# Kernel tuning notes

Hardware: AMD Instinct MI355X
Metric: run time of the kernel (lower is better)

## Reference

```python
import jax, jax.numpy as jnp
import numpy as np

B, S, D, H = 4, 4096, 1024, 16
DH = D // H


def setup_inputs() -> dict:
    key = jax.random.key(0)
    ks = jax.random.split(key, 8)
    scale = 1.0 / np.sqrt(D)
    return {
        "q": jax.random.normal(ks[0], (B, S, D), jnp.float32),
        "k": jax.random.normal(ks[1], (B, S, D), jnp.float32),
        "v": jax.random.normal(ks[2], (B, S, D), jnp.float32),
        "mask": jax.random.uniform(ks[3], (H, H), jnp.float32),
        # torch nn.Linear weights, layout [out, in]; applied as x @ W.T
        "Wq": jax.random.normal(ks[4], (D, D), jnp.float32) * scale,
        "Wk": jax.random.normal(ks[5], (D, D), jnp.float32) * scale,
        "Wv": jax.random.normal(ks[6], (D, D), jnp.float32) * scale,
        "Wo": jax.random.normal(ks[7], (D, D), jnp.float32) * scale,
    }


def reference(q, k, v, mask, Wq, Wk, Wv, Wo):
    # projections (bias-free Linear): x @ W.T, then split to [B,S,H,DH]
    qh = (q @ Wq.T).reshape(B, S, H, DH)
    kh = (k @ Wk.T).reshape(B, S, H, DH)
    vh = (v @ Wv.T).reshape(B, S, H, DH)
    # Faithful to source: NO head/seq transpose, so attention is over the
    # head axis per token: score [B,S,H,H]
    score = jnp.einsum('bshd,bsgd->bshg', qh, kh) / np.sqrt(DH)
    score = score * mask  # multiplicative mask, broadcast [H,H]
    p = jax.nn.softmax(score, axis=-1)
    attn = jnp.einsum('bshg,bsgd->bshd', p, vh)  # [B,S,H,DH]
    out = attn.reshape(B, S, D) @ Wo.T
    return out
```

## Files before the change

### kernel.cpp

```cpp
#include <hip/hip_runtime.h>
#include <hip/hip_bf16.h>
#include <stdint.h>


namespace {
constexpr int kD  = 1024;
constexpr int kH  = 16;
constexpr int kDH = 64;
constexpr int kM  = 4 * 4096;
constexpr size_t PER = (size_t)kM * kD;
constexpr size_t WSZ = (size_t)kD * kD;

typedef __attribute__((ext_vector_type(4))) float f32x4;
typedef __attribute__((ext_vector_type(8))) short s16x8;

__device__ __forceinline__ unsigned short f2b(float f) {
  uint32_t x = __builtin_bit_cast(uint32_t, f);
  x += 0x7fffu + ((x >> 16) & 1u);
  return (unsigned short)(x >> 16);
}
__device__ __forceinline__ float b2f(unsigned short u) {
  return __builtin_bit_cast(float, (uint32_t)u << 16);
}

typedef __attribute__((address_space(3))) void as3_void;
typedef __attribute__((address_space(1))) void as1_void;
__device__ __forceinline__ void gload_lds16(const void* g, void* l) {
  __builtin_amdgcn_global_load_lds((const as1_void*)(uintptr_t)g,
                                   (as3_void*)(uint32_t)(uintptr_t)l, 16, 0, 0);
}

__global__ __launch_bounds__(256) void cvt_bf16(
    const float* __restrict__ q, const float* __restrict__ k, const float* __restrict__ v,
    const float* __restrict__ Wq, const float* __restrict__ Wk, const float* __restrict__ Wv,
    const float* __restrict__ Wo, unsigned short* __restrict__ out) {
  const size_t total8 = (3 * PER + 4 * WSZ) / 8;
  for (size_t i8 = (size_t)blockIdx.x * blockDim.x + threadIdx.x; i8 < total8;
       i8 += (size_t)gridDim.x * blockDim.x) {
    size_t i = i8 * 8;
    const float* s; size_t o;
    if (i < 3 * PER) {
      if (i < PER)            { s = q; o = i; }
      else if (i < 2 * PER)   { s = k; o = i - PER; }
      else                    { s = v; o = i - 2 * PER; }
    } else {
      size_t j = i - 3 * PER;
      if (j < WSZ)            { s = Wq; o = j; }
      else if (j < 2 * WSZ)   { s = Wk; o = j - WSZ; }
      else if (j < 3 * WSZ)   { s = Wv; o = j - 2 * WSZ; }
      else                    { s = Wo; o = j - 3 * WSZ; }
    }
    f32x4 f0 = ((const f32x4*)(s + o))[0];
    f32x4 f1 = ((const f32x4*)(s + o))[1];
    s16x8 r;
#pragma unroll
    for (int d = 0; d < 4; ++d) {
      r[d]     = (short)f2b(f0[d]);
      r[4 + d] = (short)f2b(f1[d]);
    }
    *(s16x8*)(out + i) = r;
  }
}

constexpr int BM2 = 256, BN2 = 256, BK2 = 64;
constexpr int KT2 = kD / BK2;

template <bool OUT_F32>
__device__ __forceinline__ void gemm8_body(const unsigned short* __restrict__ A,
                                           const unsigned short* __restrict__ Bm,
                                           void* __restrict__ Cp) {
  constexpr int N = kD, K = kD;
  __shared__ __align__(16) unsigned short lds[65536];

  const int lin = blockIdx.y * gridDim.x + blockIdx.x;
  const int xcd = lin & 7;
  const int idx = lin >> 3;
  const int m0 = (xcd * 8 + (idx >> 2)) * BM2;
  const int n0 = (idx & 3) * BN2;

  const int t    = threadIdx.x;
  const int lane = t & 63;
  const int w    = t >> 6;
  const int wm   = w >> 2;
  const int wn   = w & 3;

  const int srow  = lane >> 3;
  const int sslot = (lane & 7) ^ srow;
  const unsigned short* gA = A  + (size_t)(m0 + w * 32 + srow) * K + sslot * 8;
  const unsigned short* gB = Bm + (size_t)(n0 + w * 32 + srow) * K + sslot * 8;

  f32x4 acc[8][4];
#pragma unroll
  for (int i = 0; i < 8; ++i)
#pragma unroll
    for (int j = 0; j < 4; ++j) acc[i][j] = (f32x4){0.f, 0.f, 0.f, 0.f};

  const int fr     = lane & 15;
  const int fkslot = lane >> 4;

  auto stage = [&](int buf, int k0) {
    const int ab = buf * 32768 + w * 2048;
    const int bb = ab + 16384;
#pragma unroll
    for (int i = 0; i < 4; ++i)
      gload_lds16(gA + k0 + (size_t)i * 8 * K, lds + ab + i * 512);
#pragma unroll
    for (int i = 0; i < 4; ++i)
      gload_lds16(gB + k0 + (size_t)i * 8 * K, lds + bb + i * 512);
  };

  auto rdA = [&](int cb, int mi, int kk) -> s16x8 {
    int ra = wm * 128 + mi * 16 + fr;
    int slot = (kk * 4 + fkslot) ^ (ra & 7);
    return *(const s16x8*)(lds + cb + ra * 64 + slot * 8);
  };
  auto rdB = [&](int cb, int nj, int kk) -> s16x8 {
    int rb = wn * 64 + nj * 16 + fr;
    int slot = (kk * 4 + fkslot) ^ (rb & 7);
    return *(const s16x8*)(lds + cb + 16384 + rb * 64 + slot * 8);
  };

  stage(0, 0);

  for (int tt = 0; tt < KT2; ++tt) {
    const int cb = (tt & 1) * 32768;
    s16x8 bw[4][2];
    if (tt + 1 < KT2) {
      stage((tt + 1) & 1, (tt + 1) * BK2);
      asm volatile("s_waitcnt vmcnt(8)" ::: "memory");
    } else {
      asm volatile("s_waitcnt vmcnt(0)" ::: "memory");
    }
    __builtin_amdgcn_s_barrier();
    {
#pragma unroll
      for (int nj = 0; nj < 4; ++nj)
#pragma unroll
        for (int kk = 0; kk < 2; ++kk) bw[nj][kk] = rdB(cb, nj, kk);
      s16x8 af[2][2];
#pragma unroll
      for (int m2 = 0; m2 < 2; ++m2)
#pragma unroll
        for (int kk = 0; kk < 2; ++kk) af[m2][kk] = rdA(cb, m2, kk);
      asm volatile("s_waitcnt lgkmcnt(0)" ::: "memory");
      __builtin_amdgcn_sched_barrier(0);
      __builtin_amdgcn_s_setprio(1);
#pragma unroll
      for (int m2 = 0; m2 < 2; ++m2)
#pragma unroll
        for (int nj = 0; nj < 4; ++nj)
#pragma unroll
          for (int kk = 0; kk < 2; ++kk)
            acc[m2][nj] =
                __builtin_amdgcn_mfma_f32_16x16x32_bf16(af[m2][kk], bw[nj][kk], acc[m2][nj], 0, 0, 0);
      __builtin_amdgcn_s_setprio(0);
    }
    __builtin_amdgcn_s_barrier();
#pragma unroll
    for (int q = 1; q < 4; ++q) {
      s16x8 af[2][2];
#pragma unroll
      for (int m2 = 0; m2 < 2; ++m2)
#pragma unroll
        for (int kk = 0; kk < 2; ++kk) af[m2][kk] = rdA(cb, q * 2 + m2, kk);
      __builtin_amdgcn_s_barrier();
      asm volatile("s_waitcnt lgkmcnt(0)" ::: "memory");
      __builtin_amdgcn_sched_barrier(0);
      __builtin_amdgcn_s_setprio(1);
#pragma unroll
      for (int m2 = 0; m2 < 2; ++m2)
#pragma unroll
        for (int nj = 0; nj < 4; ++nj)
#pragma unroll
          for (int kk = 0; kk < 2; ++kk)
            acc[q * 2 + m2][nj] =
                __builtin_amdgcn_mfma_f32_16x16x32_bf16(af[m2][kk], bw[nj][kk],
                                                        acc[q * 2 + m2][nj], 0, 0, 0);
      __builtin_amdgcn_s_setprio(0);
      __builtin_amdgcn_s_barrier();
    }
  }

  const int cr = (lane >> 4) * 4;
  const int cc = lane & 15;
#pragma unroll
  for (int mi = 0; mi < 8; ++mi)
#pragma unroll
    for (int nj = 0; nj < 4; ++nj)
#pragma unroll
      for (int r = 0; r < 4; ++r) {
        size_t row = (size_t)(m0 + wm * 128 + mi * 16 + cr + r);
        size_t col = (size_t)(n0 + wn * 64 + nj * 16 + cc);
        if constexpr (OUT_F32)
          ((float*)Cp)[row * N + col] = acc[mi][nj][r];
        else
          ((unsigned short*)Cp)[row * N + col] = f2b(acc[mi][nj][r]);
      }
}

__global__ __launch_bounds__(512, 2) void proj_gemm8(
    const unsigned short* __restrict__ qb, const unsigned short* __restrict__ kb,
    const unsigned short* __restrict__ vb, const unsigned short* __restrict__ Wqb,
    const unsigned short* __restrict__ Wkb, const unsigned short* __restrict__ Wvb,
    unsigned short* __restrict__ qh, unsigned short* __restrict__ kh,
    unsigned short* __restrict__ vh) {
  const unsigned short *A, *W;
  unsigned short* C;
  if (blockIdx.z == 0)      { A = qb; W = Wqb; C = qh; }
  else if (blockIdx.z == 1) { A = kb; W = Wkb; C = kh; }
  else                      { A = vb; W = Wvb; C = vh; }
  gemm8_body<false>(A, W, C);
}

__global__ __launch_bounds__(512, 2) void out_gemm8(const unsigned short* __restrict__ attn,
                                                    const unsigned short* __restrict__ Wob,
                                                    float* __restrict__ out) {
  gemm8_body<true>(attn, Wob, out);
}

__global__ __launch_bounds__(256) void attn_tok(const unsigned short* __restrict__ qh,
                                                const unsigned short* __restrict__ kh,
                                                const unsigned short* __restrict__ vh,
                                                const float* __restrict__ mask,
                                                unsigned short* __restrict__ attn) {
  __shared__ float P[4][16][17];
  __shared__ __align__(16) unsigned short Vs[4][16 * 64];
  const int lane = threadIdx.x & 63;
  const int wid  = threadIdx.x >> 6;
  const size_t tok = (size_t)blockIdx.x * 4 + wid;

  const unsigned short* qp = qh + tok * kD;
  const unsigned short* kp = kh + tok * kD;
  const unsigned short* vp = vh + tok * kD;

  {
    const s16x8* src = (const s16x8*)vp;
    s16x8 a = src[2 * lane], b = src[2 * lane + 1];
    s16x8* dst = (s16x8*)Vs[wid];
    dst[2 * lane] = a;
    dst[2 * lane + 1] = b;
  }

  const int fr = lane & 15;
  const int fk = (lane >> 4) * 8;
  s16x8 a0 = *(const s16x8*)(qp + fr * kDH + fk);
  s16x8 a1 = *(const s16x8*)(qp + fr * kDH + 32 + fk);
  s16x8 b0 = *(const s16x8*)(kp + fr * kDH + fk);
  s16x8 b1 = *(const s16x8*)(kp + fr * kDH + 32 + fk);
  f32x4 s = {0.f, 0.f, 0.f, 0.f};
  s = __builtin_amdgcn_mfma_f32_16x16x32_bf16(a0, b0, s, 0, 0, 0);
  s = __builtin_amdgcn_mfma_f32_16x16x32_bf16(a1, b1, s, 0, 0, 0);

  const int cr = (lane >> 4) * 4;
  const int cc = lane & 15;
  float p[4];
#pragma unroll
  for (int r = 0; r < 4; ++r) {
    float val = s[r] * 0.125f * mask[(cr + r) * kH + cc];
    float mx = val;
#pragma unroll
    for (int d = 1; d < 16; d <<= 1) mx = fmaxf(mx, __shfl_xor(mx, d));
    float e = __expf(val - mx);
    float sum = e;
#pragma unroll
    for (int d = 1; d < 16; d <<= 1) sum += __shfl_xor(sum, d);
    p[r] = e / sum;
  }
#pragma unroll
  for (int r = 0; r < 4; ++r) P[wid][cr + r][cc] = p[r];

  const int h  = lane >> 2;
  const int d0 = (lane & 3) * 16;
  float o[16];
#pragma unroll
  for (int i = 0; i < 16; ++i) o[i] = 0.f;
#pragma unroll
  for (int g = 0; g < 16; ++g) {
    float pg = P[wid][h][g];
    s16x8 v0 = *(const s16x8*)(Vs[wid] + g * kDH + d0);
    s16x8 v1 = *(const s16x8*)(Vs[wid] + g * kDH + d0 + 8);
#pragma unroll
    for (int dd = 0; dd < 8; ++dd) {
      o[dd]     += pg * b2f((unsigned short)v0[dd]);
      o[8 + dd] += pg * b2f((unsigned short)v1[dd]);
    }
  }
  unsigned short* op = attn + tok * kD + h * kDH + d0;
  s16x8 r0, r1;
#pragma unroll
  for (int dd = 0; dd < 8; ++dd) {
    r0[dd] = (short)f2b(o[dd]);
    r1[dd] = (short)f2b(o[dd + 8]);
  }
  *(s16x8*)op = r0;
  *(s16x8*)(op + 8) = r1;
}

constexpr int BM = 128, BN = 128, BK = 32;
constexpr int LDSP = BK + 8;
__device__ __forceinline__ void cvt16_store(const float* __restrict__ g, short* __restrict__ l) {
  const f32x4* s4 = (const f32x4*)g;
  f32x4 f0 = s4[0], f1 = s4[1], f2 = s4[2], f3 = s4[3];
  s16x8 o0, o1;
#pragma unroll
  for (int i = 0; i < 4; ++i) {
    o0[i]     = (short)f2b(f0[i]);
    o0[4 + i] = (short)f2b(f1[i]);
    o1[i]     = (short)f2b(f2[i]);
    o1[4 + i] = (short)f2b(f3[i]);
  }
  *(s16x8*)l = o0;
  *(s16x8*)(l + 8) = o1;
}

template <bool A_BF16, bool OUT_F32>
__device__ __forceinline__ void gemm_body_cvt(const void* __restrict__ Ap,
                                              const float* __restrict__ Wp,
                                              void* __restrict__ Cp) {
  constexpr int N = kD, K = kD;
  __shared__ short As[BM * LDSP];
  __shared__ short Bs[BN * LDSP];
  const int t  = threadIdx.x;
  const int m0 = blockIdx.y * BM;
  const int n0 = blockIdx.x * BN;
  const int srow = t >> 1;
  const int scol = (t & 1) * 16;
  const int lane = t & 63;
  const int wid  = t >> 6;
  const int wm   = (wid >> 1) * 64;
  const int wn   = (wid & 1) * 64;
  const int fr   = lane & 15;
  const int fk   = (lane >> 4) * 8;

  f32x4 acc[4][4];
#pragma unroll
  for (int i = 0; i < 4; ++i)
#pragma unroll
    for (int j = 0; j < 4; ++j) acc[i][j] = (f32x4){0.f, 0.f, 0.f, 0.f};

  for (int k0 = 0; k0 < K; k0 += BK) {
    if constexpr (A_BF16) {
      const unsigned short* Ab = (const unsigned short*)Ap;
      const s16x8* src = (const s16x8*)(Ab + (size_t)(m0 + srow) * K + k0 + scol);
      s16x8 v0 = src[0], v1 = src[1];
      *(s16x8*)(As + srow * LDSP + scol) = v0;
      *(s16x8*)(As + srow * LDSP + scol + 8) = v1;
    } else {
      cvt16_store((const float*)Ap + (size_t)(m0 + srow) * K + k0 + scol,
                  As + srow * LDSP + scol);
    }
    cvt16_store(Wp + (size_t)(n0 + srow) * K + k0 + scol, Bs + srow * LDSP + scol);
    __syncthreads();
    s16x8 af[4], bw[4];
#pragma unroll
    for (int i = 0; i < 4; ++i)
      af[i] = *(const s16x8*)(As + (wm + i * 16 + fr) * LDSP + fk);
#pragma unroll
    for (int j = 0; j < 4; ++j)
      bw[j] = *(const s16x8*)(Bs + (wn + j * 16 + fr) * LDSP + fk);
#pragma unroll
    for (int i = 0; i < 4; ++i)
#pragma unroll
      for (int j = 0; j < 4; ++j)
        acc[i][j] = __builtin_amdgcn_mfma_f32_16x16x32_bf16(af[i], bw[j], acc[i][j], 0, 0, 0);
    __syncthreads();
  }
  const int cr = (lane >> 4) * 4;
  const int cc = lane & 15;
#pragma unroll
  for (int i = 0; i < 4; ++i)
#pragma unroll
    for (int j = 0; j < 4; ++j)
#pragma unroll
      for (int r = 0; r < 4; ++r) {
        size_t row = (size_t)(m0 + wm + i * 16 + cr + r);
        size_t col = (size_t)(n0 + wn + j * 16 + cc);
        if constexpr (OUT_F32)
          ((float*)Cp)[row * N + col] = acc[i][j][r];
        else
          ((unsigned short*)Cp)[row * N + col] = f2b(acc[i][j][r]);
      }
}

__global__ __launch_bounds__(256) void proj_gemm_cvt(
    const float* __restrict__ q, const float* __restrict__ k, const float* __restrict__ v,
    const float* __restrict__ Wq, const float* __restrict__ Wk, const float* __restrict__ Wv,
    unsigned short* __restrict__ qh, unsigned short* __restrict__ kh,
    unsigned short* __restrict__ vh) {
  const float* A; const float* W; unsigned short* C;
  if (blockIdx.z == 0)      { A = q; W = Wq; C = qh; }
  else if (blockIdx.z == 1) { A = k; W = Wk; C = kh; }
  else                      { A = v; W = Wv; C = vh; }
  gemm_body_cvt<false, false>(A, W, C);
}

__global__ __launch_bounds__(256) void out_gemm_cvt(const unsigned short* __restrict__ attn,
                                                    const float* __restrict__ Wo,
                                                    float* __restrict__ out) {
  gemm_body_cvt<true, true>(attn, Wo, out);
}

}

extern "C" void kernel_launch(void* const* d_in, const int* in_sizes, int n_in,
                              void* d_out, int out_size, void* d_ws, size_t ws_size,
                              hipStream_t stream) {
  (void)in_sizes; (void)n_in; (void)out_size;
  const float* q    = (const float*)d_in[0];
  const float* k    = (const float*)d_in[1];
  const float* v    = (const float*)d_in[2];
  const float* mask = (const float*)d_in[3];
  const float* Wq   = (const float*)d_in[4];
  const float* Wk   = (const float*)d_in[5];
  const float* Wv   = (const float*)d_in[6];
  const float* Wo   = (const float*)d_in[7];

  const size_t need = (6 * PER + 4 * WSZ) * sizeof(unsigned short);
  if (ws_size >= need) {
    unsigned short* qb  = (unsigned short*)d_ws;
    unsigned short* kb  = qb + PER;
    unsigned short* vb  = kb + PER;
    unsigned short* Wqb = vb + PER;
    unsigned short* Wkb = Wqb + WSZ;
    unsigned short* Wvb = Wkb + WSZ;
    unsigned short* Wob = Wvb + WSZ;
    unsigned short* qh  = Wob + WSZ;
    unsigned short* kh  = qh + PER;
    unsigned short* vh  = kh + PER;
    unsigned short* at  = qb;

    cvt_bf16<<<2048, 256, 0, stream>>>(q, k, v, Wq, Wk, Wv, Wo, qb);
    proj_gemm8<<<dim3(kD / BN2, kM / BM2, 3), 512, 0, stream>>>(qb, kb, vb, Wqb, Wkb, Wvb,
                                                                qh, kh, vh);
    attn_tok<<<dim3(kM / 4), 256, 0, stream>>>(qh, kh, vh, mask, at);
    out_gemm8<<<dim3(kD / BN2, kM / BM2), 512, 0, stream>>>(at, Wob, (float*)d_out);
  } else {
    unsigned short* qh = (unsigned short*)d_ws;
    unsigned short* kh = qh + PER;
    unsigned short* vh = kh + PER;
    unsigned short* at = (ws_size >= 4 * PER * sizeof(unsigned short)) ? (vh + PER) : qh;
    proj_gemm_cvt<<<dim3(kD / BN, kM / BM, 3), 256, 0, stream>>>(q, k, v, Wq, Wk, Wv,
                                                                 qh, kh, vh);
    attn_tok<<<dim3(kM / 4), 256, 0, stream>>>(qh, kh, vh, mask, at);
    out_gemm_cvt<<<dim3(kD / BN, kM / BM), 256, 0, stream>>>(at, Wo, (float*)d_out);
  }
}
```

Baseline: 239.2 us.

## Fuse fp32-to-bf16 activation conversion into projection GEMM A-tile loading

The projection GEMM now reads the fp32 q/k/v activations directly. It loads each A tile into registers, converts it to bf16 and writes it into swizzled LDS, with the load for the tile after next issued ahead of time. The standalone conversion kernel now converts only the weights, which removes a full read/write pass over the activations and shrinks the workspace. The main loop is also restructured around one barrier pair per K-step instead of per-quarter barriers. In exchange, the GEMM fetches twice as many A bytes per tile and spends extra VALU work and registers on conversion, and the attention output now aliases the qh buffer.

```diff
diff --git a/kernel.cpp b/kernel.cpp
--- a/kernel.cpp
+++ b/kernel.cpp
@@ -30,26 +30,19 @@
                                    (as3_void*)(uint32_t)(uintptr_t)l, 16, 0, 0);
 }
 
-__global__ __launch_bounds__(256) void cvt_bf16(
-    const float* __restrict__ q, const float* __restrict__ k, const float* __restrict__ v,
-    const float* __restrict__ Wq, const float* __restrict__ Wk, const float* __restrict__ Wv,
-    const float* __restrict__ Wo, unsigned short* __restrict__ out) {
-  const size_t total8 = (3 * PER + 4 * WSZ) / 8;
+__global__ __launch_bounds__(256) void cvt_w(
+    const float* __restrict__ Wq, const float* __restrict__ Wk,
+    const float* __restrict__ Wv, const float* __restrict__ Wo,
+    unsigned short* __restrict__ out) {
+  const size_t total8 = 4 * WSZ / 8;
   for (size_t i8 = (size_t)blockIdx.x * blockDim.x + threadIdx.x; i8 < total8;
        i8 += (size_t)gridDim.x * blockDim.x) {
     size_t i = i8 * 8;
     const float* s; size_t o;
-    if (i < 3 * PER) {
-      if (i < PER)            { s = q; o = i; }
-      else if (i < 2 * PER)   { s = k; o = i - PER; }
-      else                    { s = v; o = i - 2 * PER; }
-    } else {
-      size_t j = i - 3 * PER;
-      if (j < WSZ)            { s = Wq; o = j; }
-      else if (j < 2 * WSZ)   { s = Wk; o = j - WSZ; }
-      else if (j < 3 * WSZ)   { s = Wv; o = j - 2 * WSZ; }
-      else                    { s = Wo; o = j - 3 * WSZ; }
-    }
+    if (i < WSZ)            { s = Wq; o = i; }
+    else if (i < 2 * WSZ)   { s = Wk; o = i - WSZ; }
+    else if (i < 3 * WSZ)   { s = Wv; o = i - 2 * WSZ; }
+    else                    { s = Wo; o = i - 3 * WSZ; }
     f32x4 f0 = ((const f32x4*)(s + o))[0];
     f32x4 f1 = ((const f32x4*)(s + o))[1];
     s16x8 r;
@@ -65,8 +58,8 @@
 constexpr int BM2 = 256, BN2 = 256, BK2 = 64;
 constexpr int KT2 = kD / BK2;
 
-template <bool OUT_F32>
-__device__ __forceinline__ void gemm8_body(const unsigned short* __restrict__ A,
+template <bool A_F32, bool OUT_F32>
+__device__ __forceinline__ void gemm8_body(const void* __restrict__ Ap,
                                            const unsigned short* __restrict__ Bm,
                                            void* __restrict__ Cp) {
   constexpr int N = kD, K = kD;
@@ -86,8 +79,11 @@
 
   const int srow  = lane >> 3;
   const int sslot = (lane & 7) ^ srow;
-  const unsigned short* gA = A  + (size_t)(m0 + w * 32 + srow) * K + sslot * 8;
   const unsigned short* gB = Bm + (size_t)(n0 + w * 32 + srow) * K + sslot * 8;
+  const unsigned short* gA_b16 =
+      A_F32 ? nullptr
+            : ((const unsigned short*)Ap + (size_t)(m0 + w * 32 + srow) * K + sslot * 8);
+  const float* Af = A_F32 ? (const float*)Ap : nullptr;
 
   f32x4 acc[8][4];
 #pragma unroll
@@ -98,12 +94,40 @@
   const int fr     = lane & 15;
   const int fkslot = lane >> 4;
 
-  auto stage = [&](int buf, int k0) {
+  f32x4 areg[8];
+
+  auto issueA = [&](int k0) {
+#pragma unroll
+    for (int i = 0; i < 4; ++i) {
+      const float* src =
+          Af + (size_t)(m0 + w * 32 + i * 8 + (lane >> 3)) * K + k0 + (lane & 7) * 8;
+      areg[2 * i]     = ((const f32x4*)src)[0];
+      areg[2 * i + 1] = ((const f32x4*)src)[1];
+    }
+  };
+  auto cvtWriteA = [&](int buf) {
+    const int base = buf * 32768;
+#pragma unroll
+    for (int i = 0; i < 4; ++i) {
+      const int row  = w * 32 + i * 8 + (lane >> 3);
+      const int slot = (lane & 7) ^ (row & 7);
+      s16x8 c;
+#pragma unroll
+      for (int d = 0; d < 4; ++d) {
+        c[d]     = (short)f2b(areg[2 * i][d]);
+        c[4 + d] = (short)f2b(areg[2 * i + 1][d]);
+      }
+      *(s16x8*)(lds + base + row * 64 + slot * 8) = c;
+    }
+  };
+  auto stageA_lds = [&](int buf, int k0) {
     const int ab = buf * 32768 + w * 2048;
-    const int bb = ab + 16384;
 #pragma unroll
     for (int i = 0; i < 4; ++i)
-      gload_lds16(gA + k0 + (size_t)i * 8 * K, lds + ab + i * 512);
+      gload_lds16(gA_b16 + k0 + (size_t)i * 8 * K, lds + ab + i * 512);
+  };
+  auto stageB = [&](int buf, int k0) {
+    const int bb = buf * 32768 + 16384 + w * 2048;
 #pragma unroll
     for (int i = 0; i < 4; ++i)
       gload_lds16(gB + k0 + (size_t)i * 8 * K, lds + bb + i * 512);
@@ -120,30 +144,54 @@
     return *(const s16x8*)(lds + cb + 16384 + rb * 64 + slot * 8);
   };
 
-  stage(0, 0);
+  if constexpr (A_F32) {
+    issueA(0);
+    cvtWriteA(0);
+    stageB(0, 0);
+    issueA(BK2);
+  } else {
+    stageA_lds(0, 0);
+    stageB(0, 0);
+  }
 
   for (int tt = 0; tt < KT2; ++tt) {
     const int cb = (tt & 1) * 32768;
+
+    __builtin_amdgcn_s_barrier();
+    if constexpr (A_F32) {
+      if (tt + 1 < KT2) {
+        stageB((tt + 1) & 1, (tt + 1) * BK2);
+        asm volatile("s_waitcnt vmcnt(12)" ::: "memory");
+        cvtWriteA((tt + 1) & 1);
+        if (tt + 2 < KT2) issueA((tt + 2) * BK2);
+      } else {
+        asm volatile("s_waitcnt vmcnt(0)" ::: "memory");
+      }
+      asm volatile("s_waitcnt lgkmcnt(0)" ::: "memory");
+    } else {
+      if (tt + 1 < KT2) {
+        stageA_lds((tt + 1) & 1, (tt + 1) * BK2);
+        stageB((tt + 1) & 1, (tt + 1) * BK2);
+        asm volatile("s_waitcnt vmcnt(8)" ::: "memory");
+      } else {
+        asm volatile("s_waitcnt vmcnt(0)" ::: "memory");
+      }
+    }
+    __builtin_amdgcn_s_barrier();
+
     s16x8 bw[4][2];
-    if (tt + 1 < KT2) {
-      stage((tt + 1) & 1, (tt + 1) * BK2);
-      asm volatile("s_waitcnt vmcnt(8)" ::: "memory");
-    } else {
-      asm volatile("s_waitcnt vmcnt(0)" ::: "memory");
-    }
-    __builtin_amdgcn_s_barrier();
-    {
-#pragma unroll
-      for (int nj = 0; nj < 4; ++nj)
-#pragma unroll
-        for (int kk = 0; kk < 2; ++kk) bw[nj][kk] = rdB(cb, nj, kk);
+#pragma unroll
+    for (int nj = 0; nj < 4; ++nj)
+#pragma unroll
+      for (int kk = 0; kk < 2; ++kk) bw[nj][kk] = rdB(cb, nj, kk);
+
+#pragma unroll
+    for (int q = 0; q < 4; ++q) {
       s16x8 af[2][2];
 #pragma unroll
       for (int m2 = 0; m2 < 2; ++m2)
 #pragma unroll
-        for (int kk = 0; kk < 2; ++kk) af[m2][kk] = rdA(cb, m2, kk);
-      asm volatile("s_waitcnt lgkmcnt(0)" ::: "memory");
-      __builtin_amdgcn_sched_barrier(0);
+        for (int kk = 0; kk < 2; ++kk) af[m2][kk] = rdA(cb, q * 2 + m2, kk);
       __builtin_amdgcn_s_setprio(1);
 #pragma unroll
       for (int m2 = 0; m2 < 2; ++m2)
@@ -151,33 +199,9 @@
         for (int nj = 0; nj < 4; ++nj)
 #pragma unroll
           for (int kk = 0; kk < 2; ++kk)
-            acc[m2][nj] =
-                __builtin_amdgcn_mfma_f32_16x16x32_bf16(af[m2][kk], bw[nj][kk], acc[m2][nj], 0, 0, 0);
+            acc[q * 2 + m2][nj] = __builtin_amdgcn_mfma_f32_16x16x32_bf16(
+                af[m2][kk], bw[nj][kk], acc[q * 2 + m2][nj], 0, 0, 0);
       __builtin_amdgcn_s_setprio(0);
-    }
-    __builtin_amdgcn_s_barrier();
-#pragma unroll
-    for (int q = 1; q < 4; ++q) {
-      s16x8 af[2][2];
-#pragma unroll
-      for (int m2 = 0; m2 < 2; ++m2)
-#pragma unroll
-        for (int kk = 0; kk < 2; ++kk) af[m2][kk] = rdA(cb, q * 2 + m2, kk);
-      __builtin_amdgcn_s_barrier();
-      asm volatile("s_waitcnt lgkmcnt(0)" ::: "memory");
-      __builtin_amdgcn_sched_barrier(0);
-      __builtin_amdgcn_s_setprio(1);
-#pragma unroll
-      for (int m2 = 0; m2 < 2; ++m2)
-#pragma unroll
-        for (int nj = 0; nj < 4; ++nj)
-#pragma unroll
-          for (int kk = 0; kk < 2; ++kk)
-            acc[q * 2 + m2][nj] =
-                __builtin_amdgcn_mfma_f32_16x16x32_bf16(af[m2][kk], bw[nj][kk],
-                                                        acc[q * 2 + m2][nj], 0, 0, 0);
-      __builtin_amdgcn_s_setprio(0);
-      __builtin_amdgcn_s_barrier();
     }
   }
 
@@ -199,23 +223,23 @@
 }
 
 __global__ __launch_bounds__(512, 2) void proj_gemm8(
-    const unsigned short* __restrict__ qb, const unsigned short* __restrict__ kb,
-    const unsigned short* __restrict__ vb, const unsigned short* __restrict__ Wqb,
-    const unsigned short* __restrict__ Wkb, const unsigned short* __restrict__ Wvb,
-    unsigned short* __restrict__ qh, unsigned short* __restrict__ kh,
-    unsigned short* __restrict__ vh) {
-  const unsigned short *A, *W;
+    const float* __restrict__ q, const float* __restrict__ k, const float* __restrict__ v,
+    const unsigned short* __restrict__ Wqb, const unsigned short* __restrict__ Wkb,
+    const unsigned short* __restrict__ Wvb, unsigned short* __restrict__ qh,
+    unsigned short* __restrict__ kh, unsigned short* __restrict__ vh) {
+  const float* A;
+  const unsigned short* W;
   unsigned short* C;
-  if (blockIdx.z == 0)      { A = qb; W = Wqb; C = qh; }
-  else if (blockIdx.z == 1) { A = kb; W = Wkb; C = kh; }
-  else                      { A = vb; W = Wvb; C = vh; }
-  gemm8_body<false>(A, W, C);
+  if (blockIdx.z == 0)      { A = q; W = Wqb; C = qh; }
+  else if (blockIdx.z == 1) { A = k; W = Wkb; C = kh; }
+  else                      { A = v; W = Wvb; C = vh; }
+  gemm8_body<true, false>(A, W, C);
 }
 
 __global__ __launch_bounds__(512, 2) void out_gemm8(const unsigned short* __restrict__ attn,
                                                     const unsigned short* __restrict__ Wob,
                                                     float* __restrict__ out) {
-  gemm8_body<true>(attn, Wob, out);
+  gemm8_body<false, true>(attn, Wob, out);
 }
 
 __global__ __launch_bounds__(256) void attn_tok(const unsigned short* __restrict__ qh,
@@ -415,22 +439,19 @@
   const float* Wv   = (const float*)d_in[6];
   const float* Wo   = (const float*)d_in[7];
 
-  const size_t need = (6 * PER + 4 * WSZ) * sizeof(unsigned short);
+  const size_t need = (3 * PER + 4 * WSZ) * sizeof(unsigned short);
   if (ws_size >= need) {
-    unsigned short* qb  = (unsigned short*)d_ws;
-    unsigned short* kb  = qb + PER;
-    unsigned short* vb  = kb + PER;
-    unsigned short* Wqb = vb + PER;
+    unsigned short* Wqb = (unsigned short*)d_ws;
     unsigned short* Wkb = Wqb + WSZ;
     unsigned short* Wvb = Wkb + WSZ;
     unsigned short* Wob = Wvb + WSZ;
     unsigned short* qh  = Wob + WSZ;
     unsigned short* kh  = qh + PER;
     unsigned short* vh  = kh + PER;
-    unsigned short* at  = qb;
-
-    cvt_bf16<<<2048, 256, 0, stream>>>(q, k, v, Wq, Wk, Wv, Wo, qb);
-    proj_gemm8<<<dim3(kD / BN2, kM / BM2, 3), 512, 0, stream>>>(qb, kb, vb, Wqb, Wkb, Wvb,
+    unsigned short* at  = qh;
+
+    cvt_w<<<256, 256, 0, stream>>>(Wq, Wk, Wv, Wo, Wqb);
+    proj_gemm8<<<dim3(kD / BN2, kM / BM2, 3), 512, 0, stream>>>(q, k, v, Wqb, Wkb, Wvb,
                                                                 qh, kh, vh);
     attn_tok<<<dim3(kM / 4), 256, 0, stream>>>(qh, kh, vh, mask, at);
     out_gemm8<<<dim3(kD / BN2, kM / BM2), 512, 0, stream>>>(at, Wob, (float*)d_out);
```

New measurement: 210.3 us. 1.14x faster.

## Restructure bf16 GEMM into four quadrant sub-tiles with half-tile staged prefetch

Applied to the files above, without the earlier changes.

The 256x256 block GEMM now splits its tile into four 128x128 quadrants, with 8 warps arranged 4x2 across each quadrant. A and B are staged in 128-row half-tiles across eight LDS slots, and the global-to-LDS loads for the next k-steps are spread between the four quadrant MFMA phases. The goal is finer-grained overlap of global loads with MFMA work and fewer full-tile waits per k-iteration. The trade-off is more barriers and more intricate vmcnt bookkeeping, which could stall or break if the counts are wrong.

```diff
diff --git a/kernel.cpp b/kernel.cpp
--- a/kernel.cpp
+++ b/kernel.cpp
@@ -65,11 +65,25 @@
 constexpr int BM2 = 256, BN2 = 256, BK2 = 64;
 constexpr int KT2 = kD / BK2;
 
+__device__ __forceinline__ void mfma16(f32x4 (&a)[2][4], s16x8 (&af)[2][2],
+                                       s16x8 (&bw)[4][2]) {
+  __builtin_amdgcn_s_setprio(1);
+#pragma unroll
+  for (int mi = 0; mi < 2; ++mi)
+#pragma unroll
+    for (int nj = 0; nj < 4; ++nj)
+#pragma unroll
+      for (int kk = 0; kk < 2; ++kk)
+        a[mi][nj] = __builtin_amdgcn_mfma_f32_16x16x32_bf16(af[mi][kk], bw[nj][kk],
+                                                            a[mi][nj], 0, 0, 0);
+  __builtin_amdgcn_s_setprio(0);
+}
+
 template <bool OUT_F32>
-__device__ __forceinline__ void gemm8_body(const unsigned short* __restrict__ A,
+__device__ __forceinline__ void gemmq_body(const unsigned short* __restrict__ A,
                                            const unsigned short* __restrict__ Bm,
                                            void* __restrict__ Cp) {
-  constexpr int N = kD, K = kD;
+  constexpr int K = kD, N = kD;
   __shared__ __align__(16) unsigned short lds[65536];
 
   const int lin = blockIdx.y * gridDim.x + blockIdx.x;
@@ -81,124 +95,128 @@
   const int t    = threadIdx.x;
   const int lane = t & 63;
   const int w    = t >> 6;
-  const int wm   = w >> 2;
-  const int wn   = w & 3;
+  const int wrow = w >> 1;
+  const int wcol = w & 1;
 
   const int srow  = lane >> 3;
   const int sslot = (lane & 7) ^ srow;
-  const unsigned short* gA = A  + (size_t)(m0 + w * 32 + srow) * K + sslot * 8;
-  const unsigned short* gB = Bm + (size_t)(n0 + w * 32 + srow) * K + sslot * 8;
-
-  f32x4 acc[8][4];
-#pragma unroll
-  for (int i = 0; i < 8; ++i)
-#pragma unroll
-    for (int j = 0; j < 4; ++j) acc[i][j] = (f32x4){0.f, 0.f, 0.f, 0.f};
-
   const int fr     = lane & 15;
   const int fkslot = lane >> 4;
 
-  auto stage = [&](int buf, int k0) {
-    const int ab = buf * 32768 + w * 2048;
-    const int bb = ab + 16384;
-#pragma unroll
-    for (int i = 0; i < 4; ++i)
-      gload_lds16(gA + k0 + (size_t)i * 8 * K, lds + ab + i * 512);
-#pragma unroll
-    for (int i = 0; i < 4; ++i)
-      gload_lds16(gB + k0 + (size_t)i * 8 * K, lds + bb + i * 512);
+  auto stageHalf = [&](const unsigned short* src, int grow0, int k0, int slot) {
+    const unsigned short* g = src + (size_t)(grow0 + w * 16 + srow) * K + k0 + sslot * 8;
+    unsigned short* l = lds + slot * 8192 + w * 16 * 64;
+    gload_lds16(g, l);
+    gload_lds16(g + (size_t)8 * K, l + 8 * 64);
   };
-
-  auto rdA = [&](int cb, int mi, int kk) -> s16x8 {
-    int ra = wm * 128 + mi * 16 + fr;
-    int slot = (kk * 4 + fkslot) ^ (ra & 7);
-    return *(const s16x8*)(lds + cb + ra * 64 + slot * 8);
+  auto rdA = [&](int slot, int mi, int kk) -> s16x8 {
+    int r = wrow * 32 + mi * 16 + fr;
+    int s16 = (kk * 4 + fkslot) ^ (r & 7);
+    return *(const s16x8*)(lds + slot * 8192 + r * 64 + s16 * 8);
   };
-  auto rdB = [&](int cb, int nj, int kk) -> s16x8 {
-    int rb = wn * 64 + nj * 16 + fr;
-    int slot = (kk * 4 + fkslot) ^ (rb & 7);
-    return *(const s16x8*)(lds + cb + 16384 + rb * 64 + slot * 8);
+  auto rdB = [&](int slot, int nj, int kk) -> s16x8 {
+    int r = wcol * 64 + nj * 16 + fr;
+    int s16 = (kk * 4 + fkslot) ^ (r & 7);
+    return *(const s16x8*)(lds + slot * 8192 + r * 64 + s16 * 8);
   };
 
-  stage(0, 0);
+  f32x4 acc[4][2][4];
+#pragma unroll
+  for (int qi = 0; qi < 4; ++qi)
+#pragma unroll
+    for (int mi = 0; mi < 2; ++mi)
+#pragma unroll
+      for (int nj = 0; nj < 4; ++nj) acc[qi][mi][nj] = (f32x4){0.f, 0.f, 0.f, 0.f};
+
+  stageHalf(A,  m0,       0, 0);
+  stageHalf(Bm, n0,       0, 2);
+  stageHalf(Bm, n0 + 128, 0, 3);
+  stageHalf(A,  m0 + 128, 0, 1);
+  stageHalf(A,  m0,       BK2, 4);
+  stageHalf(Bm, n0 + 128, BK2, 7);
+
+  s16x8 af[2][2], bw[4][2];
 
   for (int tt = 0; tt < KT2; ++tt) {
-    const int cb = (tt & 1) * 32768;
-    s16x8 bw[4][2];
+    const int b  = (tt & 1) * 4;
+    const int nb = b ^ 4;
+    const int k1 = (tt + 1) * BK2;
+    const int k2 = (tt + 2) * BK2;
+
+    if (tt == 0)            { asm volatile("s_waitcnt vmcnt(8)" ::: "memory"); }
+    else if (tt == KT2 - 1) { asm volatile("s_waitcnt vmcnt(0)" ::: "memory"); }
+    else                    { asm volatile("s_waitcnt vmcnt(4)" ::: "memory"); }
+    __builtin_amdgcn_s_barrier();
+#pragma unroll
+    for (int mi = 0; mi < 2; ++mi)
+#pragma unroll
+      for (int kk = 0; kk < 2; ++kk) af[mi][kk] = rdA(b + 0, mi, kk);
+#pragma unroll
+    for (int nj = 0; nj < 4; ++nj)
+#pragma unroll
+      for (int kk = 0; kk < 2; ++kk) bw[nj][kk] = rdB(b + 2, nj, kk);
     if (tt + 1 < KT2) {
-      stage((tt + 1) & 1, (tt + 1) * BK2);
-      asm volatile("s_waitcnt vmcnt(8)" ::: "memory");
-    } else {
-      asm volatile("s_waitcnt vmcnt(0)" ::: "memory");
+      stageHalf(A,  m0 + 128, k1, nb + 1);
+      stageHalf(Bm, n0,       k1, nb + 2);
     }
+    asm volatile("s_waitcnt lgkmcnt(0)" ::: "memory");
+    __builtin_amdgcn_sched_barrier(0);
+    mfma16(acc[0], af, bw);
+
+    if (tt == 0) { asm volatile("s_waitcnt vmcnt(8)" ::: "memory"); }
+    else         { asm volatile("s_waitcnt vmcnt(4)" ::: "memory"); }
     __builtin_amdgcn_s_barrier();
-    {
-#pragma unroll
-      for (int nj = 0; nj < 4; ++nj)
-#pragma unroll
-        for (int kk = 0; kk < 2; ++kk) bw[nj][kk] = rdB(cb, nj, kk);
-      s16x8 af[2][2];
-#pragma unroll
-      for (int m2 = 0; m2 < 2; ++m2)
-#pragma unroll
-        for (int kk = 0; kk < 2; ++kk) af[m2][kk] = rdA(cb, m2, kk);
-      asm volatile("s_waitcnt lgkmcnt(0)" ::: "memory");
-      __builtin_amdgcn_sched_barrier(0);
-      __builtin_amdgcn_s_setprio(1);
-#pragma unroll
-      for (int m2 = 0; m2 < 2; ++m2)
-#pragma unroll
-        for (int nj = 0; nj < 4; ++nj)
-#pragma unroll
-          for (int kk = 0; kk < 2; ++kk)
-            acc[m2][nj] =
-                __builtin_amdgcn_mfma_f32_16x16x32_bf16(af[m2][kk], bw[nj][kk], acc[m2][nj], 0, 0, 0);
-      __builtin_amdgcn_s_setprio(0);
-    }
+#pragma unroll
+    for (int nj = 0; nj < 4; ++nj)
+#pragma unroll
+      for (int kk = 0; kk < 2; ++kk) bw[nj][kk] = rdB(b + 3, nj, kk);
+    asm volatile("s_waitcnt lgkmcnt(0)" ::: "memory");
+    __builtin_amdgcn_sched_barrier(0);
+    mfma16(acc[1], af, bw);
+
     __builtin_amdgcn_s_barrier();
 #pragma unroll
-    for (int q = 1; q < 4; ++q) {
-      s16x8 af[2][2];
-#pragma unroll
-      for (int m2 = 0; m2 < 2; ++m2)
-#pragma unroll
-        for (int kk = 0; kk < 2; ++kk) af[m2][kk] = rdA(cb, q * 2 + m2, kk);
-      __builtin_amdgcn_s_barrier();
-      asm volatile("s_waitcnt lgkmcnt(0)" ::: "memory");
-      __builtin_amdgcn_sched_barrier(0);
-      __builtin_amdgcn_s_setprio(1);
-#pragma unroll
-      for (int m2 = 0; m2 < 2; ++m2)
-#pragma unroll
-        for (int nj = 0; nj < 4; ++nj)
-#pragma unroll
-          for (int kk = 0; kk < 2; ++kk)
-            acc[q * 2 + m2][nj] =
-                __builtin_amdgcn_mfma_f32_16x16x32_bf16(af[m2][kk], bw[nj][kk],
-                                                        acc[q * 2 + m2][nj], 0, 0, 0);
-      __builtin_amdgcn_s_setprio(0);
-      __builtin_amdgcn_s_barrier();
-    }
-  }
-
+    for (int mi = 0; mi < 2; ++mi)
+#pragma unroll
+      for (int kk = 0; kk < 2; ++kk) af[mi][kk] = rdA(b + 1, mi, kk);
+    if (tt + 2 < KT2) stageHalf(A, m0, k2, b + 0);
+    asm volatile("s_waitcnt lgkmcnt(0)" ::: "memory");
+    __builtin_amdgcn_sched_barrier(0);
+    mfma16(acc[2], af, bw);
+
+    __builtin_amdgcn_s_barrier();
+#pragma unroll
+    for (int nj = 0; nj < 4; ++nj)
+#pragma unroll
+      for (int kk = 0; kk < 2; ++kk) bw[nj][kk] = rdB(b + 2, nj, kk);
+    if (tt + 2 < KT2) stageHalf(Bm, n0 + 128, k2, b + 3);
+    asm volatile("s_waitcnt lgkmcnt(0)" ::: "memory");
+    __builtin_amdgcn_sched_barrier(0);
+    mfma16(acc[3], af, bw);
+  }
+
+  constexpr int MH[4] = {0, 0, 1, 1};
+  constexpr int NH[4] = {0, 1, 1, 0};
   const int cr = (lane >> 4) * 4;
   const int cc = lane & 15;
 #pragma unroll
-  for (int mi = 0; mi < 8; ++mi)
-#pragma unroll
-    for (int nj = 0; nj < 4; ++nj)
-#pragma unroll
-      for (int r = 0; r < 4; ++r) {
-        size_t row = (size_t)(m0 + wm * 128 + mi * 16 + cr + r);
-        size_t col = (size_t)(n0 + wn * 64 + nj * 16 + cc);
-        if constexpr (OUT_F32)
-          ((float*)Cp)[row * N + col] = acc[mi][nj][r];
-        else
-          ((unsigned short*)Cp)[row * N + col] = f2b(acc[mi][nj][r]);
-      }
-}
-
-__global__ __launch_bounds__(512, 2) void proj_gemm8(
+  for (int qi = 0; qi < 4; ++qi)
+#pragma unroll
+    for (int mi = 0; mi < 2; ++mi)
+#pragma unroll
+      for (int nj = 0; nj < 4; ++nj)
+#pragma unroll
+        for (int r = 0; r < 4; ++r) {
+          size_t row = (size_t)(m0 + MH[qi] * 128 + wrow * 32 + mi * 16 + cr + r);
+          size_t col = (size_t)(n0 + NH[qi] * 128 + wcol * 64 + nj * 16 + cc);
+          if constexpr (OUT_F32)
+            ((float*)Cp)[row * N + col] = acc[qi][mi][nj][r];
+          else
+            ((unsigned short*)Cp)[row * N + col] = f2b(acc[qi][mi][nj][r]);
+        }
+}
+
+__global__ __launch_bounds__(512, 2) void proj_gemmq(
     const unsigned short* __restrict__ qb, const unsigned short* __restrict__ kb,
     const unsigned short* __restrict__ vb, const unsigned short* __restrict__ Wqb,
     const unsigned short* __restrict__ Wkb, const unsigned short* __restrict__ Wvb,
@@ -209,13 +227,13 @@
   if (blockIdx.z == 0)      { A = qb; W = Wqb; C = qh; }
   else if (blockIdx.z == 1) { A = kb; W = Wkb; C = kh; }
   else                      { A = vb; W = Wvb; C = vh; }
-  gemm8_body<false>(A, W, C);
-}
-
-__global__ __launch_bounds__(512, 2) void out_gemm8(const unsigned short* __restrict__ attn,
+  gemmq_body<false>(A, W, C);
+}
+
+__global__ __launch_bounds__(512, 2) void out_gemmq(const unsigned short* __restrict__ attn,
                                                     const unsigned short* __restrict__ Wob,
                                                     float* __restrict__ out) {
-  gemm8_body<true>(attn, Wob, out);
+  gemmq_body<true>(attn, Wob, out);
 }
 
 __global__ __launch_bounds__(256) void attn_tok(const unsigned short* __restrict__ qh,
@@ -430,10 +448,10 @@
     unsigned short* at  = qb;
 
     cvt_bf16<<<2048, 256, 0, stream>>>(q, k, v, Wq, Wk, Wv, Wo, qb);
-    proj_gemm8<<<dim3(kD / BN2, kM / BM2, 3), 512, 0, stream>>>(qb, kb, vb, Wqb, Wkb, Wvb,
+    proj_gemmq<<<dim3(kD / BN2, kM / BM2, 3), 512, 0, stream>>>(qb, kb, vb, Wqb, Wkb, Wvb,
                                                                 qh, kh, vh);
     attn_tok<<<dim3(kM / 4), 256, 0, stream>>>(qh, kh, vh, mask, at);
-    out_gemm8<<<dim3(kD / BN2, kM / BM2), 512, 0, stream>>>(at, Wob, (float*)d_out);
+    out_gemmq<<<dim3(kD / BN2, kM / BM2), 512, 0, stream>>>(at, Wob, (float*)d_out);
   } else {
     unsigned short* qh = (unsigned short*)d_ws;
     unsigned short* kh = qh + PER;
```

Result: faster. 224.3 us (-6.2%).
